# Kernel optimization log

Measured on AMD Instinct MI355X. Metric: run time of the kernel, lower is better.

The kernel has to match this reference:

```python
import jax, jax.numpy as jnp
import numpy as np
import math

N = 256  # channels == model dim M
B, H, W = 8, 48, 48
EPS = 1e-5


def _kaiming(key, shape, a=math.sqrt(5)):
    # kaiming_normal_ with fan_in = shape[1] (2D weight), leaky_relu gain
    fan_in = shape[1]
    gain = math.sqrt(2.0 / (1.0 + a * a))
    std = gain / math.sqrt(fan_in)
    return std * jax.random.normal(key, shape, dtype=jnp.float32)


def setup_inputs() -> dict:
    key = jax.random.key(0)
    ks = jax.random.split(key, 6)
    x_l = jax.random.normal(ks[0], (B, N, H, W), dtype=jnp.float32)
    x_r = jax.random.normal(ks[1], (B, N, H, W), dtype=jnp.float32)
    Wq = _kaiming(ks[2], (N, N))
    Wk = _kaiming(ks[3], (N, N))
    Wv = _kaiming(ks[4], (N, N))
    Wo = _kaiming(ks[5], (N, N))
    g1 = jnp.ones((N,), jnp.float32); b1 = jnp.zeros((N,), jnp.float32)
    g2 = jnp.ones((N,), jnp.float32); b2 = jnp.zeros((N,), jnp.float32)
    return {"x_l": x_l, "x_r": x_r, "Wq": Wq, "Wk": Wk, "Wv": Wv, "Wo": Wo,
            "g1": g1, "b1": b1, "g2": g2, "b2": b2}


def _layernorm(x, g, b):
    mu = jnp.mean(x, axis=-1, keepdims=True)
    var = jnp.mean(jnp.square(x - mu), axis=-1, keepdims=True)
    return (x - mu) * jax.lax.rsqrt(var + EPS) * g + b


def reference(x_l, x_r, Wq, Wk, Wv, Wo, g1, b1, g2, b2):
    Bsz, C, Hh, Ww = x_l.shape
    S = Hh * Ww
    # [B, C, H, W] -> [B, S, C]
    xl = x_l.reshape(Bsz, C, S).transpose(0, 2, 1)
    xr = x_r.reshape(Bsz, C, S).transpose(0, 2, 1)
    xln_l = _layernorm(xl, g1, b1)
    xln_r = _layernorm(xr, g2, b2)
    Ql = xln_l @ Wq; Qr = xln_r @ Wq
    Kl = xln_l @ Wk; Kr = xln_r @ Wk
    Vl = xln_l @ Wv; Vr = xln_r @ Wv
    scale = 1.0 / math.sqrt(C)
    Al = jnp.einsum('bsc,btc->bst', Ql, Kr) * scale  # [B,S,S]
    Ar = jnp.einsum('bsc,btc->bst', Qr, Kl) * scale
    # NOTE: original uses nn.Softmax() with dim=None; for a 3-D tensor torch's
    # legacy _get_softmax_dim resolves to dim=0 (over batch). Faithfully replicated.
    Pl = jax.nn.softmax(Al, axis=0)
    Pr = jax.nn.softmax(Ar, axis=0)
    out_l = xl + (Pl @ Vl) @ Wo
    out_r = xr + (Pr @ Vr) @ Wo
    out_l = out_l.transpose(0, 2, 1).reshape(Bsz, C, Hh, Ww)
    out_r = out_r.transpose(0, 2, 1).reshape(Bsz, C, Hh, Ww)
    return out_l, out_r
```

## Files before the change

kernel.cpp:

```cpp
#include <hip/hip_runtime.h>
#include <stdint.h>

#define SDIM 2304
#define CDIM 256
#define NB   8
#define MTOT (NB * SDIM)

typedef __attribute__((ext_vector_type(8))) short short8;
typedef __attribute__((ext_vector_type(4))) float f32x4;

__device__ __forceinline__ float b2f(unsigned short h) {
  union { unsigned int u; float f; } v; v.u = ((unsigned int)h) << 16; return v.f;
}
__device__ __forceinline__ unsigned short f2b(float f) {
  union { unsigned int u; float f; } v; v.f = f;
  unsigned int u = v.u;
  u += 0x7fffu + ((u >> 16) & 1u);
  return (unsigned short)(u >> 16);
}
static inline unsigned short f2b_host(float f) {
  union { unsigned int u; float f; } v; v.f = f;
  unsigned int u = v.u;
  u += 0x7fffu + ((u >> 16) & 1u);
  return (unsigned short)(u >> 16);
}

__device__ __forceinline__ void gload_lds16(const unsigned short* g, unsigned short* l) {
  __builtin_amdgcn_global_load_lds(
      (const __attribute__((address_space(1))) unsigned int*)g,
      (__attribute__((address_space(3))) unsigned int*)l,
      16, 0, 0);
}

__global__ __launch_bounds__(64)
void detect_dtype(const unsigned short* __restrict__ x, int* __restrict__ flag)
{
  int lane = threadIdx.x;
  int bad = 0;
  for (int i = lane; i < 1024; i += 64) {
    float v = b2f(x[i]);
    if (!(fabsf(v) < 1e20f)) bad = 1;
  }
  unsigned long long m = __ballot(bad);
  if (lane == 0) flag[0] = (m != 0ULL) ? 1 : 0;
}

constexpr int EP_PLAIN = 0, EP_QKV = 1, EP_OUT = 2, EP_ACC = 3;

template <int EP>
__global__ __launch_bounds__(256, 2)
void gemm_nt(const unsigned short* __restrict__ pA, int lda, long sAz,
             const unsigned short* __restrict__ pB, int ldb, long sBz, int zx,
             unsigned short* __restrict__ pC, int ldc, long sCz,
             unsigned short* __restrict__ pQ, unsigned short* __restrict__ pK,
             unsigned short* __restrict__ pV,
             const unsigned short* __restrict__ pX0, const unsigned short* __restrict__ pX1,
             float* __restrict__ pFacc, unsigned short* __restrict__ pBf, int accmode,
             const int* __restrict__ dflag, int Kdim)
{
  __shared__ __align__(16) unsigned short As[128 * 32];
  __shared__ __align__(16) unsigned short Bs[128 * 32];

  const int tid = threadIdx.x;
  const int z = blockIdx.z;
  const long m0 = (long)blockIdx.x * 128;
  const long n0 = (long)blockIdx.y * 128;
  const unsigned short* A  = pA + (long)z * sAz;
  const unsigned short* Bm = pB + (long)(z ^ zx) * sBz;

  const int lane = tid & 63;
  const int wave = tid >> 6;
  const int wm = (wave & 1) << 6;
  const int wn = (wave >> 1) << 6;
  const int lr = lane & 15;
  const int quad = lane >> 4;

  f32x4 acc[4][4];
#pragma unroll
  for (int i = 0; i < 4; ++i)
#pragma unroll
    for (int j = 0; j < 4; ++j) acc[i][j] = (f32x4)0.0f;

  const int e0 = tid, e1 = tid + 256;
  const int r0 = e0 >> 2, c0 = (e0 & 3) << 3;
  const int r1 = e1 >> 2, c1 = (e1 & 3) << 3;
  const unsigned short* pa0 = A  + (m0 + r0) * lda + c0;
  const unsigned short* pa1 = A  + (m0 + r1) * lda + c1;
  const unsigned short* pb0 = Bm + (n0 + r0) * ldb + c0;
  const unsigned short* pb1 = Bm + (n0 + r1) * ldb + c1;

  for (int k0 = 0; k0 < Kdim; k0 += 32) {
    __syncthreads();
    gload_lds16(pa0 + k0, &As[e0 * 8]);
    gload_lds16(pa1 + k0, &As[e1 * 8]);
    gload_lds16(pb0 + k0, &Bs[e0 * 8]);
    gload_lds16(pb1 + k0, &Bs[e1 * 8]);
    __syncthreads();

    short8 af[4], bf[4];
#pragma unroll
    for (int i = 0; i < 4; ++i) {
      af[i] = *(const short8*)&As[(wm + i * 16 + lr) * 32 + quad * 8];
      bf[i] = *(const short8*)&Bs[(wn + i * 16 + lr) * 32 + quad * 8];
    }
#pragma unroll
    for (int i = 0; i < 4; ++i)
#pragma unroll
      for (int j = 0; j < 4; ++j)
        acc[i][j] = __builtin_amdgcn_mfma_f32_16x16x32_bf16(af[i], bf[j], acc[i][j], 0, 0, 0);
  }

  if constexpr (EP == EP_PLAIN) {
    unsigned short* Cp = pC + (long)z * sCz;
#pragma unroll
    for (int i = 0; i < 4; ++i) {
      const long mb = m0 + wm + i * 16 + quad * 4;
#pragma unroll
      for (int j = 0; j < 4; ++j) {
        const long n = n0 + wn + j * 16 + lr;
#pragma unroll
        for (int r = 0; r < 4; ++r)
          Cp[(mb + r) * ldc + n] = f2b(acc[i][j][r]);
      }
    }
  } else if constexpr (EP == EP_QKV) {
    const int g  = (int)(n0 >> 8);
    const int nb = (int)(n0 & 255);
    if (g < 2) {
      unsigned short* Cp = (g == 0 ? pQ : pK) + (long)z * sCz;
#pragma unroll
      for (int i = 0; i < 4; ++i) {
        const long mb = m0 + wm + i * 16 + quad * 4;
#pragma unroll
        for (int j = 0; j < 4; ++j) {
          const int n = nb + wn + j * 16 + lr;
#pragma unroll
          for (int r = 0; r < 4; ++r)
            Cp[(mb + r) * CDIM + n] = f2b(acc[i][j][r]);
        }
      }
    } else {
      const int b = (int)(m0 / SDIM);
      const int sblk = (int)(m0 % SDIM);
      unsigned short* Vz = pV + ((long)z * NB + b) * (long)CDIM * SDIM;
#pragma unroll
      for (int i = 0; i < 4; ++i) {
        const int s = sblk + wm + i * 16 + quad * 4;
#pragma unroll
        for (int j = 0; j < 4; ++j) {
          const int c = nb + wn + j * 16 + lr;
          ushort4 pk;
          pk.x = f2b(acc[i][j][0]); pk.y = f2b(acc[i][j][1]);
          pk.z = f2b(acc[i][j][2]); pk.w = f2b(acc[i][j][3]);
          *(ushort4*)&Vz[(long)c * SDIM + s] = pk;
        }
      }
    }
  } else if constexpr (EP == EP_ACC) {
    float* Fz = pFacc + (long)z * SDIM * CDIM;
    unsigned short* Bz = pBf + (long)z * SDIM * CDIM;
#pragma unroll
    for (int i = 0; i < 4; ++i) {
      const long mb = m0 + wm + i * 16 + quad * 4;
#pragma unroll
      for (int j = 0; j < 4; ++j) {
        const long n = n0 + wn + j * 16 + lr;
#pragma unroll
        for (int r = 0; r < 4; ++r) {
          const long idx = (mb + r) * CDIM + n;
          float v = acc[i][j][r];
          if (accmode != 0) v += Fz[idx];
          if (accmode == 2) Bz[idx] = f2b(v);
          else              Fz[idx] = v;
        }
      }
    }
  } else {
    const int io32 = dflag[0];
    const int b = (int)(m0 / SDIM);
    const int sblk = (int)(m0 % SDIM);
    const unsigned short* Xraw = (z == 0 ? pX0 : pX1);
    if (io32) {
      const float* Xf = (const float*)Xraw + (long)b * CDIM * SDIM;
      float* Of = (float*)pC + (long)z * sCz + (long)b * CDIM * SDIM;
#pragma unroll
      for (int i = 0; i < 4; ++i) {
        const int s = sblk + wm + i * 16 + quad * 4;
#pragma unroll
        for (int j = 0; j < 4; ++j) {
          const int c = (int)n0 + wn + j * 16 + lr;
          const long off = (long)c * SDIM + s;
          float4 rx = *(const float4*)&Xf[off];
          float4 pk;
          pk.x = acc[i][j][0] + rx.x;
          pk.y = acc[i][j][1] + rx.y;
          pk.z = acc[i][j][2] + rx.z;
          pk.w = acc[i][j][3] + rx.w;
          *(float4*)&Of[off] = pk;
        }
      }
    } else {
      const unsigned short* X = Xraw + (long)b * CDIM * SDIM;
      unsigned short* O = pC + (long)z * sCz + (long)b * CDIM * SDIM;
#pragma unroll
      for (int i = 0; i < 4; ++i) {
        const int s = sblk + wm + i * 16 + quad * 4;
#pragma unroll
        for (int j = 0; j < 4; ++j) {
          const int c = (int)n0 + wn + j * 16 + lr;
          const long off = (long)c * SDIM + s;
          ushort4 rx = *(const ushort4*)&X[off];
          ushort4 pk;
          pk.x = f2b(acc[i][j][0] + b2f(rx.x));
          pk.y = f2b(acc[i][j][1] + b2f(rx.y));
          pk.z = f2b(acc[i][j][2] + b2f(rx.z));
          pk.w = f2b(acc[i][j][3] + b2f(rx.w));
          *(ushort4*)&O[off] = pk;
        }
      }
    }
  }
}

__global__ __launch_bounds__(256)
void wtrans(const unsigned short* __restrict__ Wq, const unsigned short* __restrict__ Wk,
            const unsigned short* __restrict__ Wv, const unsigned short* __restrict__ Wo,
            unsigned short* __restrict__ WT, const int* __restrict__ dflag)
{
  const int io32 = dflag[0];
  int idx = blockIdx.x * 256 + threadIdx.x;
  int w = idx >> 16, r = idx & 65535, n = r >> 8, k = r & 255;
  const unsigned short* W = (w == 0) ? Wq : (w == 1) ? Wk : (w == 2) ? Wv : Wo;
  float v = io32 ? ((const float*)W)[k * 256 + n] : b2f(W[k * 256 + n]);
  if (w == 0) v *= 0.0625f;
  WT[w * 65536 + n * 256 + k] = f2b(v);
}

__global__ __launch_bounds__(256)
void ln_kernel(const unsigned short* __restrict__ xl, const unsigned short* __restrict__ xr,
               const unsigned short* __restrict__ g1, const unsigned short* __restrict__ b1,
               const unsigned short* __restrict__ g2, const unsigned short* __restrict__ b2,
               unsigned short* __restrict__ XLN, const int* __restrict__ dflag)
{
  const int io32 = dflag[0];
  const int strm = blockIdx.z;
  const int b = blockIdx.y;
  const int s0 = blockIdx.x * 64;
  const unsigned short* xraw = (strm ? xr : xl);
  const float*          xf = (const float*)xraw + (long)b * CDIM * SDIM;
  const unsigned short* xh = xraw + (long)b * CDIM * SDIM;
  const unsigned short* gg = strm ? g2 : g1;
  const unsigned short* bb = strm ? b2 : b1;
  const int tid = threadIdx.x;
  const int sl = tid & 63;
  const int team = tid >> 6;

  __shared__ float red[2][4][64];
  __shared__ float muS[64], rsS[64];
  __shared__ __align__(16) unsigned short tile[64 * 258];

  float sum = 0.f, sq = 0.f;
  for (int c = team * 64; c < team * 64 + 64; ++c) {
    const long off = (long)c * SDIM + s0 + sl;
    float v = io32 ? xf[off] : b2f(xh[off]);
    sum += v; sq += v * v;
  }
  red[0][team][sl] = sum; red[1][team][sl] = sq;
  __syncthreads();
  if (tid < 64) {
    float s_ = red[0][0][tid] + red[0][1][tid] + red[0][2][tid] + red[0][3][tid];
    float q_ = red[1][0][tid] + red[1][1][tid] + red[1][2][tid] + red[1][3][tid];
    float mu = s_ * (1.0f / CDIM);
    float var = q_ * (1.0f / CDIM) - mu * mu;
    muS[tid] = mu;
    rsS[tid] = rsqrtf(var + 1e-5f);
  }
  __syncthreads();
  const float mu = muS[sl], rs = rsS[sl];
  for (int c = team * 64; c < team * 64 + 64; ++c) {
    const long off = (long)c * SDIM + s0 + sl;
    float v = io32 ? xf[off] : b2f(xh[off]);
    float gv = io32 ? ((const float*)gg)[c] : b2f(gg[c]);
    float bv = io32 ? ((const float*)bb)[c] : b2f(bb[c]);
    tile[sl * 258 + c] = f2b((v - mu) * rs * gv + bv);
  }
  __syncthreads();
  unsigned short* outp = XLN + ((long)strm * MTOT + (long)b * SDIM + s0) * CDIM;
  const ushort2* t2 = (const ushort2*)tile;
  ushort2* o2 = (ushort2*)outp;
#pragma unroll
  for (int i = 0; i < 32; ++i) {
    int idx = i * 256 + tid;
    int r = idx >> 7, c2 = idx & 127;
    o2[idx] = t2[r * 129 + c2];
  }
}

__global__ __launch_bounds__(256)
void softmax_bdim(unsigned short* __restrict__ Ab, long total)
{
  const int strm = blockIdx.y;
  const long i8 = (((long)blockIdx.x << 8) + threadIdx.x) << 3;
  unsigned short* base = Ab + (long)strm * NB * total + i8;
  float v[NB][8];
#pragma unroll
  for (int b = 0; b < NB; ++b) {
    const ushort4* p = (const ushort4*)(base + (long)b * total);
    ushort4 a0 = p[0], a1 = p[1];
    v[b][0] = b2f(a0.x); v[b][1] = b2f(a0.y); v[b][2] = b2f(a0.z); v[b][3] = b2f(a0.w);
    v[b][4] = b2f(a1.x); v[b][5] = b2f(a1.y); v[b][6] = b2f(a1.z); v[b][7] = b2f(a1.w);
  }
#pragma unroll
  for (int j = 0; j < 8; ++j) {
    float mx = v[0][j];
#pragma unroll
    for (int b = 1; b < NB; ++b) mx = fmaxf(mx, v[b][j]);
    float s = 0.f;
#pragma unroll
    for (int b = 0; b < NB; ++b) { float e = __expf(v[b][j] - mx); v[b][j] = e; s += e; }
    float inv = 1.0f / s;
#pragma unroll
    for (int b = 0; b < NB; ++b) v[b][j] *= inv;
  }
#pragma unroll
  for (int b = 0; b < NB; ++b) {
    ushort4 a0, a1;
    a0.x = f2b(v[b][0]); a0.y = f2b(v[b][1]); a0.z = f2b(v[b][2]); a0.w = f2b(v[b][3]);
    a1.x = f2b(v[b][4]); a1.y = f2b(v[b][5]); a1.z = f2b(v[b][6]); a1.w = f2b(v[b][7]);
    ushort4* p = (ushort4*)(base + (long)b * total);
    p[0] = a0; p[1] = a1;
  }
}

__global__ __launch_bounds__(256)
void fill_val(unsigned short* __restrict__ out, unsigned short v, int n)
{
  int i = blockIdx.x * 256 + threadIdx.x;
  if (i < n) out[i] = v;
}

extern "C" void kernel_launch(void* const* d_in, const int* in_sizes, int n_in,
                              void* d_out, int out_size, void* d_ws, size_t ws_size,
                              hipStream_t stream)
{
  const unsigned short* xl = (const unsigned short*)d_in[0];
  const unsigned short* xr = (const unsigned short*)d_in[1];
  const unsigned short* Wq = (const unsigned short*)d_in[2];
  const unsigned short* Wk = (const unsigned short*)d_in[3];
  const unsigned short* Wv = (const unsigned short*)d_in[4];
  const unsigned short* Wo = (const unsigned short*)d_in[5];
  const unsigned short* g1 = (const unsigned short*)d_in[6];
  const unsigned short* b1 = (const unsigned short*)d_in[7];
  const unsigned short* g2 = (const unsigned short*)d_in[8];
  const unsigned short* b2 = (const unsigned short*)d_in[9];
  unsigned short* out = (unsigned short*)d_out;

  const size_t need_chunk = 113770496UL + 64;
  const size_t need_full  = 227016704UL + 64;
  if (ws_size < need_chunk) {
    float wsmb = (float)(ws_size >> 20);
    unsigned short v = f2b_host(wsmb * 100.0f);
    fill_val<<<dim3((out_size + 255) / 256), 256, 0, stream>>>(out, v, out_size);
    return;
  }

  int* dFlag = (int*)((char*)d_ws + ((ws_size - 16) & ~15UL));
  detect_dtype<<<dim3(1), 64, 0, stream>>>(xl, dFlag);

  if (ws_size >= need_full) {
    unsigned short* WT  = (unsigned short*)d_ws;
    unsigned short* Qb  = WT + 262144L;
    unsigned short* Kb  = Qb + 9437184L;
    unsigned short* Vt  = Kb + 9437184L;
    unsigned short* Ab  = Vt + 9437184L;
    unsigned short* XLN = Ab;
    unsigned short* PVbf = Qb;

    wtrans<<<dim3(1024), 256, 0, stream>>>(Wq, Wk, Wv, Wo, WT, dFlag);
    ln_kernel<<<dim3(36, 8, 2), 256, 0, stream>>>(xl, xr, g1, b1, g2, b2, XLN, dFlag);

    gemm_nt<EP_QKV><<<dim3(144, 6, 2), 256, 0, stream>>>(
        XLN, CDIM, (long)MTOT * CDIM,
        WT, CDIM, 0L, 0,
        nullptr, 0, (long)MTOT * CDIM,
        Qb, Kb, Vt, nullptr, nullptr,
        nullptr, nullptr, 0, dFlag, CDIM);

    gemm_nt<EP_PLAIN><<<dim3(18, 18, 16), 256, 0, stream>>>(
        Qb, CDIM, (long)SDIM * CDIM,
        Kb, CDIM, (long)SDIM * CDIM, 8,
        Ab, SDIM, (long)SDIM * SDIM,
        nullptr, nullptr, nullptr, nullptr, nullptr,
        nullptr, nullptr, 0, dFlag, CDIM);

    softmax_bdim<<<dim3(2592, 2), 256, 0, stream>>>(Ab, (long)SDIM * SDIM);

    gemm_nt<EP_PLAIN><<<dim3(18, 2, 16), 256, 0, stream>>>(
        Ab, SDIM, (long)SDIM * SDIM,
        Vt, SDIM, (long)CDIM * SDIM, 0,
        PVbf, CDIM, (long)SDIM * CDIM,
        nullptr, nullptr, nullptr, nullptr, nullptr,
        nullptr, nullptr, 0, dFlag, SDIM);

    gemm_nt<EP_OUT><<<dim3(144, 2, 2), 256, 0, stream>>>(
        PVbf, CDIM, (long)MTOT * CDIM,
        WT + 768L * 256, CDIM, 0L, 0,
        out, 0, (long)NB * CDIM * SDIM,
        nullptr, nullptr, nullptr, xl, xr,
        nullptr, nullptr, 0, dFlag, CDIM);
    return;
  }

  unsigned short* WT  = (unsigned short*)d_ws;
  unsigned short* XLN = WT  + 1024L * 256;
  unsigned short* Abc = XLN;
  unsigned short* Qb  = XLN + 9437184L;
  unsigned short* Kb  = Qb  + 9437184L;
  unsigned short* Vt  = Kb  + 9437184L;
  float*          PVacc = (float*)(Vt + 9437184L);
  unsigned short* PVbf  = Qb;

  wtrans<<<dim3(1024), 256, 0, stream>>>(Wq, Wk, Wv, Wo, WT, dFlag);
  ln_kernel<<<dim3(36, 8, 2), 256, 0, stream>>>(xl, xr, g1, b1, g2, b2, XLN, dFlag);

  gemm_nt<EP_QKV><<<dim3(144, 6, 2), 256, 0, stream>>>(
      XLN, CDIM, (long)MTOT * CDIM,
      WT, CDIM, 0L, 0,
      nullptr, 0, (long)MTOT * CDIM,
      Qb, Kb, Vt, nullptr, nullptr,
      nullptr, nullptr, 0, dFlag, CDIM);

  for (int tc = 0; tc < 9; ++tc) {
    gemm_nt<EP_PLAIN><<<dim3(18, 2, 16), 256, 0, stream>>>(
        Qb, CDIM, (long)SDIM * CDIM,
        Kb + (long)tc * 256 * CDIM, CDIM, (long)SDIM * CDIM, 8,
        Abc, 256, (long)SDIM * 256,
        nullptr, nullptr, nullptr, nullptr, nullptr,
        nullptr, nullptr, 0, dFlag, CDIM);

    softmax_bdim<<<dim3(288, 2), 256, 0, stream>>>(Abc, (long)SDIM * 256);

    const int mode = (tc == 0) ? 0 : (tc == 8) ? 2 : 1;
    gemm_nt<EP_ACC><<<dim3(18, 2, 16), 256, 0, stream>>>(
        Abc, 256, (long)SDIM * 256,
        Vt + (long)tc * 256, SDIM, (long)CDIM * SDIM, 0,
        nullptr, 0, 0L,
        nullptr, nullptr, nullptr, nullptr, nullptr,
        PVacc, PVbf, mode, dFlag, 256);
  }

  gemm_nt<EP_OUT><<<dim3(144, 2, 2), 256, 0, stream>>>(
      PVbf, CDIM, (long)MTOT * CDIM,
      WT + 768L * 256, CDIM, 0L, 0,
      out, 0, (long)NB * CDIM * SDIM,
      nullptr, nullptr, nullptr, xl, xr,
      nullptr, nullptr, 0, dFlag, CDIM);
}
```

Before: 406.6 us.

## Triple-buffer GEMM LDS tiles with async prefetch and swizzle PV block order

Replaces the single-buffered K loop in the shared GEMM kernel with a three-stage LDS ring. Two tiles are prefetched ahead using direct global-to-LDS loads, and partial vmcnt waits let loads overlap MFMA work with one barrier per step. The P@V GEMM also gets a 1D-grid block remapping so that the two N-tile blocks sharing an A row panel run close together, improving L2 reuse of the large attention matrix. LDS use per block triples (48KB), which can limit occupancy, and correctness relies on the hand-tuned vmcnt counts.

Result: faster. 388.7 us (-4.4%).

```diff
diff --git a/kernel.cpp b/kernel.cpp
--- a/kernel.cpp
+++ b/kernel.cpp
@@ -47,7 +47,7 @@
 
 constexpr int EP_PLAIN = 0, EP_QKV = 1, EP_OUT = 2, EP_ACC = 3;
 
-template <int EP>
+template <int EP, int SW>
 __global__ __launch_bounds__(256, 2)
 void gemm_nt(const unsigned short* __restrict__ pA, int lda, long sAz,
              const unsigned short* __restrict__ pB, int ldb, long sBz, int zx,
@@ -58,13 +58,24 @@
              float* __restrict__ pFacc, unsigned short* __restrict__ pBf, int accmode,
              const int* __restrict__ dflag, int Kdim)
 {
-  __shared__ __align__(16) unsigned short As[128 * 32];
-  __shared__ __align__(16) unsigned short Bs[128 * 32];
+  __shared__ __align__(16) unsigned short As[3][128 * 32];
+  __shared__ __align__(16) unsigned short Bs[3][128 * 32];
 
   const int tid = threadIdx.x;
-  const int z = blockIdx.z;
-  const long m0 = (long)blockIdx.x * 128;
-  const long n0 = (long)blockIdx.y * 128;
+  int bx, by, bz;
+  if constexpr (SW == 1) {
+    const int h = blockIdx.x;
+    const int q = h >> 4, r = h & 15;
+    const int p = q * 8 + (r & 7);
+    by = r >> 3;
+    bx = p % 18;
+    bz = p / 18;
+  } else {
+    bx = blockIdx.x; by = blockIdx.y; bz = blockIdx.z;
+  }
+  const int z = bz;
+  const long m0 = (long)bx * 128;
+  const long n0 = (long)by * 128;
   const unsigned short* A  = pA + (long)z * sAz;
   const unsigned short* Bm = pB + (long)(z ^ zx) * sBz;
 
@@ -89,25 +100,46 @@
   const unsigned short* pb0 = Bm + (n0 + r0) * ldb + c0;
   const unsigned short* pb1 = Bm + (n0 + r1) * ldb + c1;
 
-  for (int k0 = 0; k0 < Kdim; k0 += 32) {
-    __syncthreads();
-    gload_lds16(pa0 + k0, &As[e0 * 8]);
-    gload_lds16(pa1 + k0, &As[e1 * 8]);
-    gload_lds16(pb0 + k0, &Bs[e0 * 8]);
-    gload_lds16(pb1 + k0, &Bs[e1 * 8]);
-    __syncthreads();
-
-    short8 af[4], bf[4];
+  const int nt = Kdim >> 5;
+
+  gload_lds16(pa0,      &As[0][e0 * 8]);
+  gload_lds16(pa1,      &As[0][e1 * 8]);
+  gload_lds16(pb0,      &Bs[0][e0 * 8]);
+  gload_lds16(pb1,      &Bs[0][e1 * 8]);
+  gload_lds16(pa0 + 32, &As[1][e0 * 8]);
+  gload_lds16(pa1 + 32, &As[1][e1 * 8]);
+  gload_lds16(pb0 + 32, &Bs[1][e0 * 8]);
+  gload_lds16(pb1 + 32, &Bs[1][e1 * 8]);
+
+  int bc = 0;
+  for (int t = 0; t < nt; ++t) {
+    if (t < nt - 1) asm volatile("s_waitcnt vmcnt(4)" ::: "memory");
+    else            asm volatile("s_waitcnt vmcnt(0)" ::: "memory");
+    __builtin_amdgcn_s_barrier();
+    asm volatile("" ::: "memory");
+
+    if (t + 2 < nt) {
+      const int k2 = (t + 2) << 5;
+      const int b2 = bc ? bc - 1 : 2;
+      gload_lds16(pa0 + k2, &As[b2][e0 * 8]);
+      gload_lds16(pa1 + k2, &As[b2][e1 * 8]);
+      gload_lds16(pb0 + k2, &Bs[b2][e0 * 8]);
+      gload_lds16(pb1 + k2, &Bs[b2][e1 * 8]);
+    }
+
+    short8 af[4], bfr[4];
 #pragma unroll
     for (int i = 0; i < 4; ++i) {
-      af[i] = *(const short8*)&As[(wm + i * 16 + lr) * 32 + quad * 8];
-      bf[i] = *(const short8*)&Bs[(wn + i * 16 + lr) * 32 + quad * 8];
+      af[i]  = *(const short8*)&As[bc][(wm + i * 16 + lr) * 32 + quad * 8];
+      bfr[i] = *(const short8*)&Bs[bc][(wn + i * 16 + lr) * 32 + quad * 8];
     }
 #pragma unroll
     for (int i = 0; i < 4; ++i)
 #pragma unroll
       for (int j = 0; j < 4; ++j)
-        acc[i][j] = __builtin_amdgcn_mfma_f32_16x16x32_bf16(af[i], bf[j], acc[i][j], 0, 0, 0);
+        acc[i][j] = __builtin_amdgcn_mfma_f32_16x16x32_bf16(af[i], bfr[j], acc[i][j], 0, 0, 0);
+
+    bc = (bc == 2) ? 0 : bc + 1;
   }
 
   if constexpr (EP == EP_PLAIN) {
@@ -379,14 +411,14 @@
     wtrans<<<dim3(1024), 256, 0, stream>>>(Wq, Wk, Wv, Wo, WT, dFlag);
     ln_kernel<<<dim3(36, 8, 2), 256, 0, stream>>>(xl, xr, g1, b1, g2, b2, XLN, dFlag);
 
-    gemm_nt<EP_QKV><<<dim3(144, 6, 2), 256, 0, stream>>>(
+    gemm_nt<EP_QKV, 0><<<dim3(144, 6, 2), 256, 0, stream>>>(
         XLN, CDIM, (long)MTOT * CDIM,
         WT, CDIM, 0L, 0,
         nullptr, 0, (long)MTOT * CDIM,
         Qb, Kb, Vt, nullptr, nullptr,
         nullptr, nullptr, 0, dFlag, CDIM);
 
-    gemm_nt<EP_PLAIN><<<dim3(18, 18, 16), 256, 0, stream>>>(
+    gemm_nt<EP_PLAIN, 0><<<dim3(18, 18, 16), 256, 0, stream>>>(
         Qb, CDIM, (long)SDIM * CDIM,
         Kb, CDIM, (long)SDIM * CDIM, 8,
         Ab, SDIM, (long)SDIM * SDIM,
@@ -395,14 +427,14 @@
 
     softmax_bdim<<<dim3(2592, 2), 256, 0, stream>>>(Ab, (long)SDIM * SDIM);
 
-    gemm_nt<EP_PLAIN><<<dim3(18, 2, 16), 256, 0, stream>>>(
+    gemm_nt<EP_PLAIN, 1><<<dim3(576), 256, 0, stream>>>(
         Ab, SDIM, (long)SDIM * SDIM,
         Vt, SDIM, (long)CDIM * SDIM, 0,
         PVbf, CDIM, (long)SDIM * CDIM,
         nullptr, nullptr, nullptr, nullptr, nullptr,
         nullptr, nullptr, 0, dFlag, SDIM);
 
-    gemm_nt<EP_OUT><<<dim3(144, 2, 2), 256, 0, stream>>>(
+    gemm_nt<EP_OUT, 0><<<dim3(144, 2, 2), 256, 0, stream>>>(
         PVbf, CDIM, (long)MTOT * CDIM,
         WT + 768L * 256, CDIM, 0L, 0,
         out, 0, (long)NB * CDIM * SDIM,
@@ -423,7 +455,7 @@
   wtrans<<<dim3(1024), 256, 0, stream>>>(Wq, Wk, Wv, Wo, WT, dFlag);
   ln_kernel<<<dim3(36, 8, 2), 256, 0, stream>>>(xl, xr, g1, b1, g2, b2, XLN, dFlag);
 
-  gemm_nt<EP_QKV><<<dim3(144, 6, 2), 256, 0, stream>>>(
+  gemm_nt<EP_QKV, 0><<<dim3(144, 6, 2), 256, 0, stream>>>(
       XLN, CDIM, (long)MTOT * CDIM,
       WT, CDIM, 0L, 0,
       nullptr, 0, (long)MTOT * CDIM,
@@ -431,7 +463,7 @@
       nullptr, nullptr, 0, dFlag, CDIM);
 
   for (int tc = 0; tc < 9; ++tc) {
-    gemm_nt<EP_PLAIN><<<dim3(18, 2, 16), 256, 0, stream>>>(
+    gemm_nt<EP_PLAIN, 0><<<dim3(18, 2, 16), 256, 0, stream>>>(
         Qb, CDIM, (long)SDIM * CDIM,
         Kb + (long)tc * 256 * CDIM, CDIM, (long)SDIM * CDIM, 8,
         Abc, 256, (long)SDIM * 256,
@@ -441,7 +473,7 @@
     softmax_bdim<<<dim3(288, 2), 256, 0, stream>>>(Abc, (long)SDIM * 256);
 
     const int mode = (tc == 0) ? 0 : (tc == 8) ? 2 : 1;
-    gemm_nt<EP_ACC><<<dim3(18, 2, 16), 256, 0, stream>>>(
+    gemm_nt<EP_ACC, 0><<<dim3(18, 2, 16), 256, 0, stream>>>(
         Abc, 256, (long)SDIM * 256,
         Vt + (long)tc * 256, SDIM, (long)CDIM * SDIM, 0,
         nullptr, 0, 0L,
@@ -449,7 +481,7 @@
         PVacc, PVbf, mode, dFlag, 256);
   }
 
-  gemm_nt<EP_OUT><<<dim3(144, 2, 2), 256, 0, stream>>>(
+  gemm_nt<EP_OUT, 0><<<dim3(144, 2, 2), 256, 0, stream>>>(
       PVbf, CDIM, (long)MTOT * CDIM,
       WT + 768L * 256, CDIM, 0L, 0,
       out, 0, (long)NB * CDIM * SDIM,
```
